# Kernel optimization log

Measured on AMD Instinct MI355X. Metric: run time of the kernel, lower is better.

## Reference

```python
import jax, jax.numpy as jnp
import numpy as np

B, V, H, W = 8192, 256, 128, 128  # batch, feature dim, SOM grid height/width


def setup_inputs() -> dict:
    key = jax.random.key(0)
    k1, k2 = jax.random.split(key)
    inp = jax.random.uniform(k1, (B, V), dtype=jnp.float32)
    weights = jax.random.uniform(k2, (H * W, V), dtype=jnp.float32)  # SOM codebook
    # grid node coordinates, row-major [i, j] as in the torch locations list
    ii, jj = jnp.meshgrid(jnp.arange(H), jnp.arange(W), indexing='ij')
    locations = jnp.stack([ii, jj], axis=-1).reshape(H * W, 2).astype(jnp.float32)
    return {"input": inp, "weights": weights, "locations": locations}


def reference(input, weights, locations):
    # Pairwise L2 distance between input [B,V] and codebook [N,V] via the
    x2 = jnp.sum(input * input, axis=-1, keepdims=True)        # [B,1]
    w2 = jnp.sum(weights * weights, axis=-1)                   # [N]
    d2 = x2 - 2.0 * (input @ weights.T) + w2                   # [B,N]
    dist = jnp.sqrt(jnp.maximum(d2, 0.0))
    bmu_idx = jnp.argmin(dist, axis=-1)                        # [B]
    losses = jnp.min(dist, axis=-1)                            # [B]
    bmu_locations = locations[bmu_idx]                         # [B,2]
    return bmu_locations, losses
```

## Files before the change

kernel.cpp:

```cpp
#include <hip/hip_runtime.h>
#include <stdint.h>


#define B_DIM 8192
#define V_DIM 256
#define N_DIM 16384
#define WS_W2_BYTES 65536

typedef __attribute__((ext_vector_type(8))) short short8;
typedef __attribute__((ext_vector_type(4))) float f32x4;

__device__ __forceinline__ unsigned long long packKey(float s, unsigned idx) {
    unsigned u = __float_as_uint(s);
    u = (u & 0x80000000u) ? ~u : (u | 0x80000000u);
    return ((unsigned long long)u << 32) | (unsigned long long)idx;
}

__global__ __launch_bounds__(256) void w2_kernel(const float* __restrict__ W,
                                                 float* __restrict__ w2) {
    int lane = threadIdx.x & 63;
    int wv   = threadIdx.x >> 6;
    int n    = blockIdx.x * 4 + wv;
    float4 v = ((const float4*)(W + (size_t)n * V_DIM))[lane];
    float s = v.x * v.x + v.y * v.y + v.z * v.z + v.w * v.w;
    #pragma unroll
    for (int m = 32; m >= 1; m >>= 1) s += __shfl_xor(s, m);
    if (lane == 0) w2[n] = s;
}

__device__ __forceinline__ unsigned packhi2(float a, float b) {
    return (__float_as_uint(a) >> 16) | (__float_as_uint(b) & 0xFFFF0000u);
}
__device__ __forceinline__ unsigned packlo2(float a, float b) {
    float ah = __uint_as_float(__float_as_uint(a) & 0xFFFF0000u);
    float bh = __uint_as_float(__float_as_uint(b) & 0xFFFF0000u);
    return (__float_as_uint(a - ah) >> 16) | (__float_as_uint(b - bh) & 0xFFFF0000u);
}
__device__ __forceinline__ uint4 mku4(unsigned a, unsigned b, unsigned c, unsigned d) {
    uint4 r; r.x = a; r.y = b; r.z = c; r.w = d; return r;
}
__device__ __forceinline__ uint4 hi8(float4 p, float4 q) {
    return mku4(packhi2(p.x, p.y), packhi2(p.z, p.w), packhi2(q.x, q.y), packhi2(q.z, q.w));
}
__device__ __forceinline__ uint4 lo8(float4 p, float4 q) {
    return mku4(packlo2(p.x, p.y), packlo2(p.z, p.w), packlo2(q.x, q.y), packlo2(q.z, q.w));
}

__device__ __forceinline__ int lb(int row, int slot) {
    return row * 64 + ((slot ^ ((row >> 1) & 3)) << 4);
}

#define BM 128
#define BN 128
#define BK 32
#define KSTEPS (V_DIM / BK)

__global__ __launch_bounds__(256, 2) void som_mfma(const float* __restrict__ X,
                                                   const float* __restrict__ W,
                                                   const float* __restrict__ w2,
                                                   unsigned long long* __restrict__ packed) {
    __shared__ char lds[4 * 8192];
    char* Ahi = lds;
    char* Alo = lds + 8192;
    char* Bhi = lds + 16384;
    char* Blo = lds + 24576;

    const int t     = threadIdx.x;
    const int lane  = t & 63;
    const int wv    = t >> 6;
    const int wr    = wv >> 1, wc = wv & 1;
    const int fr    = lane & 15;
    const int kslot = lane >> 4;

    const int rb = blockIdx.x >> 7;
    const int cb = blockIdx.x & 127;
    const int r0 = rb * BM, c0 = cb * BN;

    const int sr = t >> 1;
    const int sh = t & 1;
    const float* xg = X + (size_t)(r0 + sr) * V_DIM + sh * 16;
    const float* wg = W + (size_t)(c0 + sr) * V_DIM + sh * 16;

    float4 pa[4], pb[4];
    #pragma unroll
    for (int q = 0; q < 4; ++q) {
        pa[q] = ((const float4*)xg)[q];
        pb[q] = ((const float4*)wg)[q];
    }

    f32x4 acc[4][4];
    #pragma unroll
    for (int i = 0; i < 4; ++i)
        #pragma unroll
        for (int j = 0; j < 4; ++j)
            acc[i][j] = (f32x4){0.f, 0.f, 0.f, 0.f};

    for (int ks = 0; ks < KSTEPS; ++ks) {
        uint4 cah0 = hi8(pa[0], pa[1]), cah1 = hi8(pa[2], pa[3]);
        uint4 cal0 = lo8(pa[0], pa[1]), cal1 = lo8(pa[2], pa[3]);
        uint4 cbh0 = hi8(pb[0], pb[1]), cbh1 = hi8(pb[2], pb[3]);
        uint4 cbl0 = lo8(pb[0], pb[1]), cbl1 = lo8(pb[2], pb[3]);

        __syncthreads();
        *(uint4*)(Ahi + lb(sr, 2 * sh))     = cah0;
        *(uint4*)(Ahi + lb(sr, 2 * sh + 1)) = cah1;
        *(uint4*)(Alo + lb(sr, 2 * sh))     = cal0;
        *(uint4*)(Alo + lb(sr, 2 * sh + 1)) = cal1;
        *(uint4*)(Bhi + lb(sr, 2 * sh))     = cbh0;
        *(uint4*)(Bhi + lb(sr, 2 * sh + 1)) = cbh1;
        *(uint4*)(Blo + lb(sr, 2 * sh))     = cbl0;
        *(uint4*)(Blo + lb(sr, 2 * sh + 1)) = cbl1;
        __syncthreads();

        if (ks + 1 < KSTEPS) {
            const float* xn = xg + (ks + 1) * BK;
            const float* wn = wg + (ks + 1) * BK;
            #pragma unroll
            for (int q = 0; q < 4; ++q) {
                pa[q] = ((const float4*)xn)[q];
                pb[q] = ((const float4*)wn)[q];
            }
        }

        short8 fah[4], fal[4], fbh[4], fbl[4];
        #pragma unroll
        for (int i = 0; i < 4; ++i) {
            int row = wr * 64 + i * 16 + fr;
            fah[i] = *(const short8*)(Ahi + lb(row, kslot));
            fal[i] = *(const short8*)(Alo + lb(row, kslot));
        }
        #pragma unroll
        for (int j = 0; j < 4; ++j) {
            int col = wc * 64 + j * 16 + fr;
            fbh[j] = *(const short8*)(Bhi + lb(col, kslot));
            fbl[j] = *(const short8*)(Blo + lb(col, kslot));
        }
        #pragma unroll
        for (int i = 0; i < 4; ++i)
            #pragma unroll
            for (int j = 0; j < 4; ++j) {
                acc[i][j] = __builtin_amdgcn_mfma_f32_16x16x32_bf16(fah[i], fbh[j], acc[i][j], 0, 0, 0);
                acc[i][j] = __builtin_amdgcn_mfma_f32_16x16x32_bf16(fah[i], fbl[j], acc[i][j], 0, 0, 0);
                acc[i][j] = __builtin_amdgcn_mfma_f32_16x16x32_bf16(fal[i], fbh[j], acc[i][j], 0, 0, 0);
            }
    }

    float w2v[4];
    #pragma unroll
    for (int j = 0; j < 4; ++j) w2v[j] = w2[c0 + wc * 64 + j * 16 + fr];

    #pragma unroll
    for (int i = 0; i < 4; ++i) {
        #pragma unroll
        for (int r = 0; r < 4; ++r) {
            const int row = r0 + wr * 64 + i * 16 + kslot * 4 + r;
            float best = 3.4e38f;
            unsigned bidx = 0u;
            #pragma unroll
            for (int j = 0; j < 4; ++j) {
                const unsigned n = (unsigned)(c0 + wc * 64 + j * 16 + fr);
                const float s = fmaf(-2.0f, acc[i][j][r], w2v[j]);
                if (s < best) { best = s; bidx = n; }
            }
            #pragma unroll
            for (int m = 1; m <= 8; m <<= 1) {
                float    ov = __shfl_xor(best, m);
                unsigned oi = (unsigned)__shfl_xor((int)bidx, m);
                if (ov < best || (ov == best && oi < bidx)) { best = ov; bidx = oi; }
            }
            if (fr == 0) atomicMin(&packed[row], packKey(best, bidx));
        }
    }
}

__global__ __launch_bounds__(256) void finalize(const float* __restrict__ X,
                                                const float* __restrict__ loc,
                                                const unsigned long long* __restrict__ packed,
                                                float* __restrict__ out) {
    int lane = threadIdx.x & 63;
    int wv   = threadIdx.x >> 6;
    int b    = blockIdx.x * 4 + wv;
    float4 v = ((const float4*)(X + (size_t)b * V_DIM))[lane];
    float x2 = v.x * v.x + v.y * v.y + v.z * v.z + v.w * v.w;
    #pragma unroll
    for (int m = 32; m >= 1; m >>= 1) x2 += __shfl_xor(x2, m);
    if (lane == 0) {
        unsigned long long p = packed[b];
        unsigned key = (unsigned)(p >> 32);
        unsigned idx = (unsigned)(p & 0xFFFFFFFFu);
        unsigned sb  = (key & 0x80000000u) ? (key & 0x7FFFFFFFu) : ~key;
        float s  = __uint_as_float(sb);
        float d2 = fmaxf(x2 + s, 0.0f);
        out[2 * b]     = loc[2 * idx];
        out[2 * b + 1] = loc[2 * idx + 1];
        out[2 * B_DIM + b] = sqrtf(d2);
    }
}

extern "C" void kernel_launch(void* const* d_in, const int* in_sizes, int n_in,
                              void* d_out, int out_size, void* d_ws, size_t ws_size,
                              hipStream_t stream) {
    const float* X = (const float*)d_in[0];
    const float* W = (const float*)d_in[1];
    const float* L = (const float*)d_in[2];
    float* out = (float*)d_out;

    float* w2 = (float*)d_ws;
    unsigned long long* packed = (unsigned long long*)((char*)d_ws + WS_W2_BYTES);

    hipMemsetAsync(packed, 0xFF, B_DIM * sizeof(unsigned long long), stream);
    w2_kernel<<<N_DIM / 4, 256, 0, stream>>>(W, w2);
    som_mfma<<<(B_DIM / BM) * (N_DIM / BN), 256, 0, stream>>>(X, W, w2, packed);
    finalize<<<B_DIM / 4, 256, 0, stream>>>(X, L, packed, out);
}
```

Before: 312.6 us.

## Pre-split inputs into bf16 hi/lo planes and stream tiles via global_load_lds

Adds a preprocessing kernel that splits X and W once into swizzled bf16 high and low planes in workspace, rounding to nearest. A new GEMM kernel then loads those planes straight into LDS with global_load_lds. This removes the per-block fp32-to-bf16 split and the register-staged LDS stores that every tile repeated. In exchange it adds an extra pass over both inputs (about 25 MB of writes), depends on the workspace being large enough (otherwise the old kernel runs), and drops the occupancy hint from launch bounds.

```diff
diff --git a/kernel.cpp b/kernel.cpp
--- a/kernel.cpp
+++ b/kernel.cpp
@@ -5,7 +5,13 @@
 #define B_DIM 8192
 #define V_DIM 256
 #define N_DIM 16384
-#define WS_W2_BYTES 65536
+
+#define WS_W2_OFF     0
+#define WS_PACKED_OFF 65536
+#define WS_PLANES_OFF 131072
+#define XPLANE_BYTES  (B_DIM * V_DIM * 2)
+#define WPLANE_BYTES  (N_DIM * V_DIM * 2)
+#define WS_FAST_NEED  (WS_PLANES_OFF + 2 * XPLANE_BYTES + 2 * WPLANE_BYTES)
 
 typedef __attribute__((ext_vector_type(8))) short short8;
 typedef __attribute__((ext_vector_type(4))) float f32x4;
@@ -28,6 +34,173 @@
     if (lane == 0) w2[n] = s;
 }
 
+
+__device__ __forceinline__ unsigned bfrn(float x) {
+    unsigned u = __float_as_uint(x);
+    return (u + 0x7FFFu + ((u >> 16) & 1u)) >> 16;
+}
+__device__ __forceinline__ float bf2f(unsigned h) { return __uint_as_float(h << 16); }
+
+__global__ __launch_bounds__(256) void convert_planes(const float* __restrict__ X,
+                                                      const float* __restrict__ W,
+                                                      unsigned short* __restrict__ Xh,
+                                                      unsigned short* __restrict__ Xl,
+                                                      unsigned short* __restrict__ Wh,
+                                                      unsigned short* __restrict__ Wl) {
+    int gid = blockIdx.x * 256 + threadIdx.x;
+    int s   = gid & 31;
+    int row = gid >> 5;
+    const float* src;
+    unsigned short *dh, *dl;
+    int r;
+    if (row < B_DIM) { r = row; src = X + (size_t)r * V_DIM; dh = Xh; dl = Xl; }
+    else             { r = row - B_DIM; src = W + (size_t)r * V_DIM; dh = Wh; dl = Wl; }
+
+    float4 a = ((const float4*)src)[s * 2];
+    float4 b = ((const float4*)src)[s * 2 + 1];
+    float v[8] = {a.x, a.y, a.z, a.w, b.x, b.y, b.z, b.w};
+    unsigned hi[8], lo[8];
+    #pragma unroll
+    for (int i = 0; i < 8; ++i) {
+        hi[i] = bfrn(v[i]);
+        lo[i] = bfrn(v[i] - bf2f(hi[i]));
+    }
+    uint4 hp, lp;
+    hp.x = hi[0] | (hi[1] << 16); hp.y = hi[2] | (hi[3] << 16);
+    hp.z = hi[4] | (hi[5] << 16); hp.w = hi[6] | (hi[7] << 16);
+    lp.x = lo[0] | (lo[1] << 16); lp.y = lo[2] | (lo[3] << 16);
+    lp.z = lo[4] | (lo[5] << 16); lp.w = lo[6] | (lo[7] << 16);
+
+    int sp = (s & ~3) | ((s & 3) ^ ((r >> 1) & 3));
+    *(uint4*)(dh + (size_t)r * V_DIM + sp * 8) = hp;
+    *(uint4*)(dl + (size_t)r * V_DIM + sp * 8) = lp;
+}
+
+__device__ __forceinline__ void gl16(const void* g, void* l) {
+    __builtin_amdgcn_global_load_lds((const __attribute__((address_space(1))) unsigned int*)g,
+                                     (__attribute__((address_space(3))) unsigned int*)l,
+                                     16, 0, 0);
+}
+
+#define BM 128
+#define BN 128
+#define FBK 32
+#define FKSTEPS (V_DIM / FBK)
+
+__global__ __launch_bounds__(256) void som_fast(const unsigned short* __restrict__ Xh,
+                                                const unsigned short* __restrict__ Xl,
+                                                const unsigned short* __restrict__ Wh,
+                                                const unsigned short* __restrict__ Wl,
+                                                const float* __restrict__ w2,
+                                                unsigned long long* __restrict__ packed) {
+    __shared__ char lds[32768];
+    char* Ah = lds;
+    char* Al = lds + 8192;
+    char* Bh = lds + 16384;
+    char* Bl = lds + 24576;
+
+    const int t    = threadIdx.x;
+    const int lane = t & 63;
+    const int wv   = t >> 6;
+    const int wr   = wv >> 1, wc = wv & 1;
+    const int fr   = lane & 15;
+    const int kq   = lane >> 4;
+
+    const int rb = blockIdx.x >> 7;
+    const int cb = blockIdx.x & 127;
+    const int r0 = rb * BM, c0 = cb * BN;
+
+    const size_t aOff = (size_t)(r0 + (t >> 2)) * V_DIM + (t & 3) * 8;
+    const size_t bOff = (size_t)(c0 + (t >> 2)) * V_DIM + (t & 3) * 8;
+    const unsigned short* sXh = Xh + aOff;
+    const unsigned short* sXl = Xl + aOff;
+    const unsigned short* sWh = Wh + bOff;
+    const unsigned short* sWl = Wl + bOff;
+    const int t16 = t * 16;
+
+#define ISSUE(ks)                                                          \
+    do {                                                                   \
+        gl16(sXh + (ks) * FBK,            Ah + t16);                       \
+        gl16(sXh + 64 * V_DIM + (ks) * FBK, Ah + 4096 + t16);              \
+        gl16(sXl + (ks) * FBK,            Al + t16);                       \
+        gl16(sXl + 64 * V_DIM + (ks) * FBK, Al + 4096 + t16);              \
+        gl16(sWh + (ks) * FBK,            Bh + t16);                       \
+        gl16(sWh + 64 * V_DIM + (ks) * FBK, Bh + 4096 + t16);              \
+        gl16(sWl + (ks) * FBK,            Bl + t16);                       \
+        gl16(sWl + 64 * V_DIM + (ks) * FBK, Bl + 4096 + t16);              \
+    } while (0)
+
+    f32x4 acc[4][4];
+    #pragma unroll
+    for (int i = 0; i < 4; ++i)
+        #pragma unroll
+        for (int j = 0; j < 4; ++j)
+            acc[i][j] = (f32x4){0.f, 0.f, 0.f, 0.f};
+
+    ISSUE(0);
+
+    for (int ks = 0; ks < FKSTEPS; ++ks) {
+        __syncthreads();
+
+        short8 fah[4], fal[4], fbh[4], fbl[4];
+        #pragma unroll
+        for (int i = 0; i < 4; ++i) {
+            const int row = wr * 64 + i * 16 + fr;
+            const int off = row * 64 + ((kq ^ ((row >> 1) & 3)) << 4);
+            fah[i] = *(const short8*)(Ah + off);
+            fal[i] = *(const short8*)(Al + off);
+        }
+        #pragma unroll
+        for (int j = 0; j < 4; ++j) {
+            const int col = wc * 64 + j * 16 + fr;
+            const int off = col * 64 + ((kq ^ ((col >> 1) & 3)) << 4);
+            fbh[j] = *(const short8*)(Bh + off);
+            fbl[j] = *(const short8*)(Bl + off);
+        }
+        __syncthreads();
+
+        if (ks + 1 < FKSTEPS) ISSUE(ks + 1);
+
+        #pragma unroll
+        for (int i = 0; i < 4; ++i)
+            #pragma unroll
+            for (int j = 0; j < 4; ++j) {
+                acc[i][j] = __builtin_amdgcn_mfma_f32_16x16x32_bf16(fah[i], fbh[j], acc[i][j], 0, 0, 0);
+                acc[i][j] = __builtin_amdgcn_mfma_f32_16x16x32_bf16(fah[i], fbl[j], acc[i][j], 0, 0, 0);
+                acc[i][j] = __builtin_amdgcn_mfma_f32_16x16x32_bf16(fal[i], fbh[j], acc[i][j], 0, 0, 0);
+            }
+    }
+#undef ISSUE
+
+    float w2v[4];
+    #pragma unroll
+    for (int j = 0; j < 4; ++j) w2v[j] = w2[c0 + wc * 64 + j * 16 + fr];
+
+    #pragma unroll
+    for (int i = 0; i < 4; ++i) {
+        #pragma unroll
+        for (int r = 0; r < 4; ++r) {
+            const int row = r0 + wr * 64 + i * 16 + kq * 4 + r;
+            float best = 3.4e38f;
+            unsigned bidx = 0u;
+            #pragma unroll
+            for (int j = 0; j < 4; ++j) {
+                const unsigned n = (unsigned)(c0 + wc * 64 + j * 16 + fr);
+                const float s = fmaf(-2.0f, acc[i][j][r], w2v[j]);
+                if (s < best) { best = s; bidx = n; }
+            }
+            #pragma unroll
+            for (int m = 1; m <= 8; m <<= 1) {
+                float    ov = __shfl_xor(best, m);
+                unsigned oi = (unsigned)__shfl_xor((int)bidx, m);
+                if (ov < best || (ov == best && oi < bidx)) { best = ov; bidx = oi; }
+            }
+            if (fr == 0) atomicMin(&packed[row], packKey(best, bidx));
+        }
+    }
+}
+
+
 __device__ __forceinline__ unsigned packhi2(float a, float b) {
     return (__float_as_uint(a) >> 16) | (__float_as_uint(b) & 0xFFFF0000u);
 }
@@ -45,25 +218,19 @@
 __device__ __forceinline__ uint4 lo8(float4 p, float4 q) {
     return mku4(packlo2(p.x, p.y), packlo2(p.z, p.w), packlo2(q.x, q.y), packlo2(q.z, q.w));
 }
-
 __device__ __forceinline__ int lb(int row, int slot) {
     return row * 64 + ((slot ^ ((row >> 1) & 3)) << 4);
 }
-
-#define BM 128
-#define BN 128
-#define BK 32
-#define KSTEPS (V_DIM / BK)
 
 __global__ __launch_bounds__(256, 2) void som_mfma(const float* __restrict__ X,
                                                    const float* __restrict__ W,
                                                    const float* __restrict__ w2,
                                                    unsigned long long* __restrict__ packed) {
     __shared__ char lds[4 * 8192];
-    char* Ahi = lds;
-    char* Alo = lds + 8192;
-    char* Bhi = lds + 16384;
-    char* Blo = lds + 24576;
+    char* Ahp = lds;
+    char* Alp = lds + 8192;
+    char* Bhp = lds + 16384;
+    char* Blp = lds + 24576;
 
     const int t     = threadIdx.x;
     const int lane  = t & 63;
@@ -78,62 +245,55 @@
 
     const int sr = t >> 1;
     const int sh = t & 1;
-    const float* xg = X + (size_t)(r0 + sr) * V_DIM + sh * 16;
-    const float* wg = W + (size_t)(c0 + sr) * V_DIM + sh * 16;
+    const float* xg = (const float*)X + (size_t)(r0 + sr) * V_DIM + sh * 16;
+    const float* wg = (const float*)W + (size_t)(c0 + sr) * V_DIM + sh * 16;
 
     float4 pa[4], pb[4];
     #pragma unroll
-    for (int q = 0; q < 4; ++q) {
-        pa[q] = ((const float4*)xg)[q];
-        pb[q] = ((const float4*)wg)[q];
-    }
+    for (int q = 0; q < 4; ++q) { pa[q] = ((const float4*)xg)[q]; pb[q] = ((const float4*)wg)[q]; }
 
     f32x4 acc[4][4];
     #pragma unroll
     for (int i = 0; i < 4; ++i)
         #pragma unroll
-        for (int j = 0; j < 4; ++j)
-            acc[i][j] = (f32x4){0.f, 0.f, 0.f, 0.f};
-
-    for (int ks = 0; ks < KSTEPS; ++ks) {
+        for (int j = 0; j < 4; ++j) acc[i][j] = (f32x4){0.f, 0.f, 0.f, 0.f};
+
+    for (int ks = 0; ks < 8; ++ks) {
         uint4 cah0 = hi8(pa[0], pa[1]), cah1 = hi8(pa[2], pa[3]);
         uint4 cal0 = lo8(pa[0], pa[1]), cal1 = lo8(pa[2], pa[3]);
         uint4 cbh0 = hi8(pb[0], pb[1]), cbh1 = hi8(pb[2], pb[3]);
         uint4 cbl0 = lo8(pb[0], pb[1]), cbl1 = lo8(pb[2], pb[3]);
 
         __syncthreads();
-        *(uint4*)(Ahi + lb(sr, 2 * sh))     = cah0;
-        *(uint4*)(Ahi + lb(sr, 2 * sh + 1)) = cah1;
-        *(uint4*)(Alo + lb(sr, 2 * sh))     = cal0;
-        *(uint4*)(Alo + lb(sr, 2 * sh + 1)) = cal1;
-        *(uint4*)(Bhi + lb(sr, 2 * sh))     = cbh0;
-        *(uint4*)(Bhi + lb(sr, 2 * sh + 1)) = cbh1;
-        *(uint4*)(Blo + lb(sr, 2 * sh))     = cbl0;
-        *(uint4*)(Blo + lb(sr, 2 * sh + 1)) = cbl1;
+        *(uint4*)(Ahp + lb(sr, 2 * sh))     = cah0;
+        *(uint4*)(Ahp + lb(sr, 2 * sh + 1)) = cah1;
+        *(uint4*)(Alp + lb(sr, 2 * sh))     = cal0;
+        *(uint4*)(Alp + lb(sr, 2 * sh + 1)) = cal1;
+        *(uint4*)(Bhp + lb(sr, 2 * sh))     = cbh0;
+        *(uint4*)(Bhp + lb(sr, 2 * sh + 1)) = cbh1;
+        *(uint4*)(Blp + lb(sr, 2 * sh))     = cbl0;
+        *(uint4*)(Blp + lb(sr, 2 * sh + 1)) = cbl1;
         __syncthreads();
 
-        if (ks + 1 < KSTEPS) {
-            const float* xn = xg + (ks + 1) * BK;
-            const float* wn = wg + (ks + 1) * BK;
-            #pragma unroll
-            for (int q = 0; q < 4; ++q) {
-                pa[q] = ((const float4*)xn)[q];
-                pb[q] = ((const float4*)wn)[q];
-            }
+        if (ks + 1 < 8) {
+            const float* xn = xg + (ks + 1) * 32;
+            const float* wn = wg + (ks + 1) * 32;
+            #pragma unroll
+            for (int q = 0; q < 4; ++q) { pa[q] = ((const float4*)xn)[q]; pb[q] = ((const float4*)wn)[q]; }
         }
 
         short8 fah[4], fal[4], fbh[4], fbl[4];
         #pragma unroll
         for (int i = 0; i < 4; ++i) {
             int row = wr * 64 + i * 16 + fr;
-            fah[i] = *(const short8*)(Ahi + lb(row, kslot));
-            fal[i] = *(const short8*)(Alo + lb(row, kslot));
+            fah[i] = *(const short8*)(Ahp + lb(row, kslot));
+            fal[i] = *(const short8*)(Alp + lb(row, kslot));
         }
         #pragma unroll
         for (int j = 0; j < 4; ++j) {
             int col = wc * 64 + j * 16 + fr;
-            fbh[j] = *(const short8*)(Bhi + lb(col, kslot));
-            fbl[j] = *(const short8*)(Blo + lb(col, kslot));
+            fbh[j] = *(const short8*)(Bhp + lb(col, kslot));
+            fbl[j] = *(const short8*)(Blp + lb(col, kslot));
         }
         #pragma unroll
         for (int i = 0; i < 4; ++i)
@@ -205,11 +365,21 @@
     const float* L = (const float*)d_in[2];
     float* out = (float*)d_out;
 
-    float* w2 = (float*)d_ws;
-    unsigned long long* packed = (unsigned long long*)((char*)d_ws + WS_W2_BYTES);
+    float* w2 = (float*)((char*)d_ws + WS_W2_OFF);
+    unsigned long long* packed = (unsigned long long*)((char*)d_ws + WS_PACKED_OFF);
 
     hipMemsetAsync(packed, 0xFF, B_DIM * sizeof(unsigned long long), stream);
     w2_kernel<<<N_DIM / 4, 256, 0, stream>>>(W, w2);
-    som_mfma<<<(B_DIM / BM) * (N_DIM / BN), 256, 0, stream>>>(X, W, w2, packed);
+
+    if (ws_size >= (size_t)WS_FAST_NEED) {
+        unsigned short* Xh = (unsigned short*)((char*)d_ws + WS_PLANES_OFF);
+        unsigned short* Xl = (unsigned short*)((char*)Xh + XPLANE_BYTES);
+        unsigned short* Wh = (unsigned short*)((char*)Xl + XPLANE_BYTES);
+        unsigned short* Wl = (unsigned short*)((char*)Wh + WPLANE_BYTES);
+        convert_planes<<<(B_DIM + N_DIM) * 32 / 256, 256, 0, stream>>>(X, W, Xh, Xl, Wh, Wl);
+        som_fast<<<(B_DIM / BM) * (N_DIM / BN), 256, 0, stream>>>(Xh, Xl, Wh, Wl, w2, packed);
+    } else {
+        som_mfma<<<(B_DIM / BM) * (N_DIM / BN), 256, 0, stream>>>(X, W, w2, packed);
+    }
     finalize<<<B_DIM / 4, 256, 0, stream>>>(X, L, packed, out);
 }
```

After: 286.8 us. -8.3%, faster.
